# Kernel tuning notes

Hardware: AMD Instinct MI355X
Metric: run time of the kernel (lower is better)

Reference implementation:

```python
import jax, jax.numpy as jnp
import numpy as np

NUM_CLASSES = 172
IGNORE_INDEX = 255
DICE_WEIGHT = 0.5
EPS = 1e-7


def setup_inputs() -> dict:
    key = jax.random.key(0)
    k1, k2 = jax.random.split(key)
    pred = jax.random.normal(k1, (4, NUM_CLASSES, 256, 256), dtype=jnp.float32)
    target = jax.random.randint(k2, (4, 256, 256), 0, NUM_CLASSES, dtype=jnp.int32)
    return {"pred": pred, "target": target}


def reference(pred, target):
    # pred: [B, C, H, W] logits; target: [B, H, W] int labels (255 = ignore)
    C = NUM_CLASSES
    logp = jax.nn.log_softmax(pred, axis=1)  # [B, C, H, W]

    # ---- cross entropy with ignore_index (mean over valid pixels) ----
    valid = target != IGNORE_INDEX  # [B, H, W]
    safe_tgt = jnp.where(valid, target, 0)
    nll = -jnp.take_along_axis(logp, safe_tgt[:, None].astype(jnp.int32), axis=1)[:, 0]  # [B, H, W]
    n_valid = jnp.sum(valid)
    ce = jnp.sum(jnp.where(valid, nll, 0.0)) / jnp.maximum(n_valid, 1).astype(pred.dtype)

    # ---- dice loss: vectorized over classes (replaces per-class python loop) ----
    p = jnp.exp(logp)  # softmax probs [B, C, H, W]
    # intersection[c] = sum over pixels with target==c of p[:, c] at those pixels
    gathered = jnp.take_along_axis(p, safe_tgt[:, None].astype(jnp.int32), axis=1)[:, 0]  # [B, H, W]
    seg_ids = target.ravel().astype(jnp.int32)  # ignore pixels land in bucket 255, discarded
    inter = jax.ops.segment_sum(gathered.ravel(), seg_ids, num_segments=256)[:C]  # [C]
    counts = jax.ops.segment_sum(jnp.ones_like(gathered.ravel()), seg_ids, num_segments=256)[:C]
    union = jnp.sum(p, axis=(0, 2, 3)) + counts  # [C]
    valid_c = union > 0
    dice_terms = jnp.where(valid_c, (2.0 * inter + EPS) / (union + EPS), 0.0)
    n_valid_c = jnp.sum(valid_c).astype(pred.dtype)
    dice = jnp.where(n_valid_c > 0, 1.0 - jnp.sum(dice_terms) / jnp.maximum(n_valid_c, 1.0), 0.0)

    return ce + DICE_WEIGHT * dice
```

## Files before the change

kernel.cpp:

```cpp
#include <hip/hip_runtime.h>
#include <stdint.h>

#define NCLS 172
#define IGN 255
#define HW 65536
#define NPIX 262144
#define EPSV 1e-7f
#define NSTAGE 8
#define SSTRIDE 348

__device__ __forceinline__ float waveReduceSum(float v) {
    #pragma unroll
    for (int off = 32; off > 0; off >>= 1) v += __shfl_down(v, off, 64);
    return v;
}

__global__ __launch_bounds__(256) void seg_pass1(
    const float* __restrict__ pred, const int* __restrict__ tgt,
    float* __restrict__ wArr, float* __restrict__ part)
{
    __shared__ float ldsInter[NCLS];
    __shared__ unsigned int ldsCnt[NCLS];
    __shared__ float ldsRed[8];

    const int tid = threadIdx.x;
    for (int i = tid; i < NCLS; i += 256) { ldsInter[i] = 0.f; ldsCnt[i] = 0u; }
    __syncthreads();

    const int pix = blockIdx.x * 256 + tid;
    const int b  = pix >> 16;
    const int hw = pix & (HW - 1);
    const float* base = pred + (size_t)b * NCLS * HW + hw;

    const int t = tgt[pix];
    const bool valid = (t != IGN);
    const int st = valid ? t : 0;

    float s0 = 0.f, s1 = 0.f, s2 = 0.f, s3 = 0.f;
    #pragma unroll 4
    for (int c = 0; c < NCLS; c += 4) {
        float x0 = base[(size_t)(c    ) * HW];
        float x1 = base[(size_t)(c + 1) * HW];
        float x2 = base[(size_t)(c + 2) * HW];
        float x3 = base[(size_t)(c + 3) * HW];
        s0 += __expf(x0); s1 += __expf(x1); s2 += __expf(x2); s3 += __expf(x3);
    }
    const float s = (s0 + s1) + (s2 + s3);
    const float invs = 1.0f / s;
    wArr[pix] = invs;

    const float xt  = base[(size_t)st * HW];
    const float nll = valid ? (__logf(s) - xt) : 0.f;
    const float pt  = __expf(xt) * invs;
    if (valid) {
        atomicAdd(&ldsInter[st], pt);
        atomicAdd(&ldsCnt[st], 1u);
    }

    float vr = waveReduceSum(nll);
    float nr = waveReduceSum(valid ? 1.f : 0.f);
    const int wave = tid >> 6, lane = tid & 63;
    if (lane == 0) { ldsRed[wave] = vr; ldsRed[4 + wave] = nr; }
    __syncthreads();

    float* pb = part + (size_t)(blockIdx.x & (NSTAGE - 1)) * SSTRIDE;
    for (int i = tid; i < NCLS; i += 256) {
        float vi = ldsInter[i];
        if (vi != 0.f) atomicAdd(&pb[i], vi);
        unsigned int ci = ldsCnt[i];
        if (ci != 0u) atomicAdd(&pb[NCLS + i], (float)ci);
    }
    if (tid == 0) atomicAdd(&pb[344], ldsRed[0] + ldsRed[1] + ldsRed[2] + ldsRed[3]);
    if (tid == 1) atomicAdd(&pb[345], ldsRed[4] + ldsRed[5] + ldsRed[6] + ldsRed[7]);
}

__global__ __launch_bounds__(256) void seg_pass2(
    const float* __restrict__ pred, const float* __restrict__ wArr,
    float* __restrict__ g_union)
{
    const int bx = blockIdx.x;
    const int plane = bx >> 2;
    const int chunk = bx & 3;
    const int c = plane % NCLS;
    const int b = plane / NCLS;
    const float4* __restrict__ x = (const float4*)(pred + (size_t)plane * HW + chunk * 16384);
    const float4* __restrict__ w = (const float4*)(wArr + (size_t)b * HW + chunk * 16384);

    const int tid = threadIdx.x;
    float acc = 0.f;
    #pragma unroll 4
    for (int j = 0; j < 16; ++j) {
        float4 xv = x[j * 256 + tid];
        float4 wv = w[j * 256 + tid];
        acc += __expf(xv.x) * wv.x + __expf(xv.y) * wv.y
             + __expf(xv.z) * wv.z + __expf(xv.w) * wv.w;
    }

    __shared__ float red[4];
    float v = waveReduceSum(acc);
    const int wave = tid >> 6, lane = tid & 63;
    if (lane == 0) red[wave] = v;
    __syncthreads();
    if (tid == 0) atomicAdd(&g_union[c], red[0] + red[1] + red[2] + red[3]);
}

__global__ __launch_bounds__(256) void seg_fin(
    const float* __restrict__ g_union, const float* __restrict__ part,
    float* __restrict__ out)
{
    __shared__ float sT[256], sN[256];
    const int tid = threadIdx.x;
    float term = 0.f, nv = 0.f;
    if (tid < NCLS) {
        float inter = 0.f, cnt = 0.f;
        #pragma unroll
        for (int st = 0; st < NSTAGE; ++st) {
            inter += part[st * SSTRIDE + tid];
            cnt   += part[st * SSTRIDE + NCLS + tid];
        }
        float u = g_union[tid] + cnt;
        if (u > 0.f) { term = (2.f * inter + EPSV) / (u + EPSV); nv = 1.f; }
    }
    sT[tid] = term; sN[tid] = nv;
    __syncthreads();
    #pragma unroll
    for (int s2 = 128; s2 > 0; s2 >>= 1) {
        if (tid < s2) { sT[tid] += sT[tid + s2]; sN[tid] += sN[tid + s2]; }
        __syncthreads();
    }
    if (tid == 0) {
        float ce = 0.f, nvl = 0.f;
        #pragma unroll
        for (int st = 0; st < NSTAGE; ++st) {
            ce  += part[st * SSTRIDE + 344];
            nvl += part[st * SSTRIDE + 345];
        }
        float ceo  = ce / fmaxf(nvl, 1.f);
        float dice = (sN[0] > 0.f) ? (1.f - sT[0] / fmaxf(sN[0], 1.f)) : 0.f;
        out[0] = ceo + 0.5f * dice;
    }
}

extern "C" void kernel_launch(void* const* d_in, const int* in_sizes, int n_in,
                              void* d_out, int out_size, void* d_ws, size_t ws_size,
                              hipStream_t stream) {
    const float* pred = (const float*)d_in[0];
    const int*   tgt  = (const int*)d_in[1];
    float* out = (float*)d_out;

    char* ws = (char*)d_ws;
    float* g_union = (float*)ws;
    float* part    = (float*)(ws + 1024);
    float* wArr    = (float*)(ws + 16384);

    hipMemsetAsync(d_ws, 0, 16384, stream);
    seg_pass1<<<NPIX / 256, 256, 0, stream>>>(pred, tgt, wArr, part);
    seg_pass2<<<(NPIX / 16384) * NCLS, 256, 0, stream>>>(pred, wArr, g_union);
    seg_fin<<<1, 256, 0, stream>>>(g_union, part, out);
}
```

Before: 277.4 us.

## Fuse softmax-sum and union passes into one LDS-tiled kernel

Merges the two passes over pred into a single kernel. Each block stages 64 pixels by 172 classes into LDS using global_load_lds, computes per-pixel softmax sums, the CE and intersection terms, and per-class union sums from the staged tile. This reads pred from HBM once instead of twice and drops the wArr intermediate and one launch. In exchange it adds large LDS usage per block (about 44KB, so lower occupancy), several barriers per tile, and one global atomic per class per block for the union.

New measurement: 260.1 us. 6.2% less time.

```diff
diff --git a/kernel.cpp b/kernel.cpp
--- a/kernel.cpp
+++ b/kernel.cpp
@@ -6,8 +6,11 @@
 #define HW 65536
 #define NPIX 262144
 #define EPSV 1e-7f
-#define NSTAGE 8
-#define SSTRIDE 348
+#define TP 64
+#define NTILE 4
+#define PIXPERBLK (TP * NTILE)
+#define NSTAGE 16
+#define SS 520
 
 __device__ __forceinline__ float waveReduceSum(float v) {
     #pragma unroll
@@ -15,110 +18,118 @@
     return v;
 }
 
-__global__ __launch_bounds__(256) void seg_pass1(
+__device__ __forceinline__ void gl_lds16(const float* g, float* l) {
+    __builtin_amdgcn_global_load_lds(
+        (const __attribute__((address_space(1))) void*)g,
+        (__attribute__((address_space(3))) void*)l, 16, 0, 0);
+}
+
+__global__ __launch_bounds__(256) void seg_fused(
     const float* __restrict__ pred, const int* __restrict__ tgt,
-    float* __restrict__ wArr, float* __restrict__ part)
+    float* __restrict__ part)
 {
-    __shared__ float ldsInter[NCLS];
-    __shared__ unsigned int ldsCnt[NCLS];
-    __shared__ float ldsRed[8];
+    __shared__ float tile[NCLS * TP];
+    __shared__ float sPart[256];
+    __shared__ float sInvs[TP];
+    __shared__ float sInter[NCLS];
+    __shared__ unsigned int sCnt[NCLS];
 
-    const int tid = threadIdx.x;
-    for (int i = tid; i < NCLS; i += 256) { ldsInter[i] = 0.f; ldsCnt[i] = 0u; }
-    __syncthreads();
+    const int tid  = threadIdx.x;
+    const int lane = tid & 63;
+    const int wv   = tid >> 6;
+    const int p    = lane;
+    const int q    = wv;
 
-    const int pix = blockIdx.x * 256 + tid;
-    const int b  = pix >> 16;
-    const int hw = pix & (HW - 1);
-    const float* base = pred + (size_t)b * NCLS * HW + hw;
+    for (int i = tid; i < NCLS; i += 256) { sInter[i] = 0.f; sCnt[i] = 0u; }
 
-    const int t = tgt[pix];
-    const bool valid = (t != IGN);
-    const int st = valid ? t : 0;
+    const int pix0 = blockIdx.x * PIXPERBLK;
+    const int b    = pix0 >> 16;
+    const int hw0  = pix0 & (HW - 1);
+    const float* gb = pred + (size_t)b * NCLS * HW + hw0;
 
-    float s0 = 0.f, s1 = 0.f, s2 = 0.f, s3 = 0.f;
-    #pragma unroll 4
-    for (int c = 0; c < NCLS; c += 4) {
-        float x0 = base[(size_t)(c    ) * HW];
-        float x1 = base[(size_t)(c + 1) * HW];
-        float x2 = base[(size_t)(c + 2) * HW];
-        float x3 = base[(size_t)(c + 3) * HW];
-        s0 += __expf(x0); s1 += __expf(x1); s2 += __expf(x2); s3 += __expf(x3);
-    }
-    const float s = (s0 + s1) + (s2 + s3);
-    const float invs = 1.0f / s;
-    wArr[pix] = invs;
+    const int lc = lane >> 4;
+    const int lp = (lane & 15) << 2;
 
-    const float xt  = base[(size_t)st * HW];
-    const float nll = valid ? (__logf(s) - xt) : 0.f;
-    const float pt  = __expf(xt) * invs;
-    if (valid) {
-        atomicAdd(&ldsInter[st], pt);
-        atomicAdd(&ldsCnt[st], 1u);
+    float unionAcc = 0.f;
+    float ceAcc = 0.f, nvAcc = 0.f;
+
+    for (int tI = 0; tI < NTILE; ++tI) {
+        const float* gt = gb + tI * TP;
+        for (int cb = wv * 4; cb < NCLS; cb += 16)
+            gl_lds16(gt + (size_t)(cb + lc) * HW + lp, &tile[cb * TP]);
+        __syncthreads();
+
+        const int c0 = q * 43;
+        float s0 = 0.f, s1 = 0.f;
+        #pragma unroll
+        for (int i = 0; i < 42; i += 2) {
+            s0 += __expf(tile[(c0 + i    ) * TP + p]);
+            s1 += __expf(tile[(c0 + i + 1) * TP + p]);
+        }
+        s0 += __expf(tile[(c0 + 42) * TP + p]);
+        sPart[tid] = s0 + s1;
+        __syncthreads();
+
+        if (tid < 64) {
+            const float s    = (sPart[p] + sPart[64 + p]) + (sPart[128 + p] + sPart[192 + p]);
+            const float invs = 1.0f / s;
+            sInvs[p] = invs;
+            const int  t     = tgt[pix0 + tI * TP + p];
+            const bool valid = (t != IGN);
+            const int  st    = valid ? t : 0;
+            const float xt   = tile[st * TP + p];
+            const float nll  = valid ? (__logf(s) - xt) : 0.f;
+            if (valid) {
+                atomicAdd(&sInter[st], __expf(xt) * invs);
+                atomicAdd(&sCnt[st], 1u);
+            }
+            const float vr = waveReduceSum(nll);
+            const float nr = waveReduceSum(valid ? 1.f : 0.f);
+            if (lane == 0) { ceAcc += vr; nvAcc += nr; }
+        }
+        __syncthreads();
+
+        if (tid < NCLS) {
+            const int c = tid;
+            float u0 = 0.f, u1 = 0.f;
+            #pragma unroll 4
+            for (int k = 0; k < TP; k += 2) {
+                const int p0 = (c + k    ) & (TP - 1);
+                const int p1 = (c + k + 1) & (TP - 1);
+                u0 += __expf(tile[c * TP + p0]) * sInvs[p0];
+                u1 += __expf(tile[c * TP + p1]) * sInvs[p1];
+            }
+            unionAcc += u0 + u1;
+        }
+        __syncthreads();
     }
 
-    float vr = waveReduceSum(nll);
-    float nr = waveReduceSum(valid ? 1.f : 0.f);
-    const int wave = tid >> 6, lane = tid & 63;
-    if (lane == 0) { ldsRed[wave] = vr; ldsRed[4 + wave] = nr; }
-    __syncthreads();
-
-    float* pb = part + (size_t)(blockIdx.x & (NSTAGE - 1)) * SSTRIDE;
+    float* pb = part + (size_t)(blockIdx.x & (NSTAGE - 1)) * SS;
     for (int i = tid; i < NCLS; i += 256) {
-        float vi = ldsInter[i];
+        const float vi = sInter[i];
         if (vi != 0.f) atomicAdd(&pb[i], vi);
-        unsigned int ci = ldsCnt[i];
+        const unsigned int ci = sCnt[i];
         if (ci != 0u) atomicAdd(&pb[NCLS + i], (float)ci);
     }
-    if (tid == 0) atomicAdd(&pb[344], ldsRed[0] + ldsRed[1] + ldsRed[2] + ldsRed[3]);
-    if (tid == 1) atomicAdd(&pb[345], ldsRed[4] + ldsRed[5] + ldsRed[6] + ldsRed[7]);
-}
-
-__global__ __launch_bounds__(256) void seg_pass2(
-    const float* __restrict__ pred, const float* __restrict__ wArr,
-    float* __restrict__ g_union)
-{
-    const int bx = blockIdx.x;
-    const int plane = bx >> 2;
-    const int chunk = bx & 3;
-    const int c = plane % NCLS;
-    const int b = plane / NCLS;
-    const float4* __restrict__ x = (const float4*)(pred + (size_t)plane * HW + chunk * 16384);
-    const float4* __restrict__ w = (const float4*)(wArr + (size_t)b * HW + chunk * 16384);
-
-    const int tid = threadIdx.x;
-    float acc = 0.f;
-    #pragma unroll 4
-    for (int j = 0; j < 16; ++j) {
-        float4 xv = x[j * 256 + tid];
-        float4 wv = w[j * 256 + tid];
-        acc += __expf(xv.x) * wv.x + __expf(xv.y) * wv.y
-             + __expf(xv.z) * wv.z + __expf(xv.w) * wv.w;
-    }
-
-    __shared__ float red[4];
-    float v = waveReduceSum(acc);
-    const int wave = tid >> 6, lane = tid & 63;
-    if (lane == 0) red[wave] = v;
-    __syncthreads();
-    if (tid == 0) atomicAdd(&g_union[c], red[0] + red[1] + red[2] + red[3]);
+    if (tid < NCLS) atomicAdd(&pb[344 + tid], unionAcc);
+    if (tid == 0) { atomicAdd(&pb[516], ceAcc); atomicAdd(&pb[517], nvAcc); }
 }
 
 __global__ __launch_bounds__(256) void seg_fin(
-    const float* __restrict__ g_union, const float* __restrict__ part,
-    float* __restrict__ out)
+    const float* __restrict__ part, float* __restrict__ out)
 {
     __shared__ float sT[256], sN[256];
     const int tid = threadIdx.x;
     float term = 0.f, nv = 0.f;
     if (tid < NCLS) {
-        float inter = 0.f, cnt = 0.f;
+        float inter = 0.f, cnt = 0.f, uni = 0.f;
         #pragma unroll
         for (int st = 0; st < NSTAGE; ++st) {
-            inter += part[st * SSTRIDE + tid];
-            cnt   += part[st * SSTRIDE + NCLS + tid];
+            inter += part[st * SS + tid];
+            cnt   += part[st * SS + NCLS + tid];
+            uni   += part[st * SS + 344 + tid];
         }
-        float u = g_union[tid] + cnt;
+        const float u = uni + cnt;
         if (u > 0.f) { term = (2.f * inter + EPSV) / (u + EPSV); nv = 1.f; }
     }
     sT[tid] = term; sN[tid] = nv;
@@ -132,11 +143,11 @@
         float ce = 0.f, nvl = 0.f;
         #pragma unroll
         for (int st = 0; st < NSTAGE; ++st) {
-            ce  += part[st * SSTRIDE + 344];
-            nvl += part[st * SSTRIDE + 345];
+            ce  += part[st * SS + 516];
+            nvl += part[st * SS + 517];
         }
-        float ceo  = ce / fmaxf(nvl, 1.f);
-        float dice = (sN[0] > 0.f) ? (1.f - sT[0] / fmaxf(sN[0], 1.f)) : 0.f;
+        const float ceo  = ce / fmaxf(nvl, 1.f);
+        const float dice = (sN[0] > 0.f) ? (1.f - sT[0] / fmaxf(sN[0], 1.f)) : 0.f;
         out[0] = ceo + 0.5f * dice;
     }
 }
@@ -146,15 +157,10 @@
                               hipStream_t stream) {
     const float* pred = (const float*)d_in[0];
     const int*   tgt  = (const int*)d_in[1];
-    float* out = (float*)d_out;
+    float* out  = (float*)d_out;
+    float* part = (float*)d_ws;
 
-    char* ws = (char*)d_ws;
-    float* g_union = (float*)ws;
-    float* part    = (float*)(ws + 1024);
-    float* wArr    = (float*)(ws + 16384);
-
-    hipMemsetAsync(d_ws, 0, 16384, stream);
-    seg_pass1<<<NPIX / 256, 256, 0, stream>>>(pred, tgt, wArr, part);
-    seg_pass2<<<(NPIX / 16384) * NCLS, 256, 0, stream>>>(pred, wArr, g_union);
-    seg_fin<<<1, 256, 0, stream>>>(g_union, part, out);
+    hipMemsetAsync(d_ws, 0, NSTAGE * SS * sizeof(float), stream);
+    seg_fused<<<NPIX / PIXPERBLK, 256, 0, stream>>>(pred, tgt, part);
+    seg_fin<<<1, 256, 0, stream>>>(part, out);
 }
```
